# Kernel tuning notes

Hardware: AMD Instinct MI355X
Metric: run time of the kernel (lower is better)

## Reference

```python
import jax, jax.numpy as jnp
import numpy as np
import math


def _conv2d(x, w, b):
    # 3x3, stride 1, pad 1, NCHW / OIHW
    y = jax.lax.conv_general_dilated(x, w, (1, 1), ((1, 1), (1, 1)),
                                     dimension_numbers=('NCHW', 'OIHW', 'NCHW'))
    return y + b[None, :, None, None]


def _avgpool2(x):
    B, C, H, W = x.shape
    return x.reshape(B, C, H // 2, 2, W // 2, 2).mean(axis=(3, 5))


def setup_inputs() -> dict:
    key = jax.random.key(0)
    ks = jax.random.split(key, 12)
    B, H, W = 8, 512, 512
    x = jax.random.uniform(ks[0], (B, 3, H, W), dtype=jnp.float32)

    def conv_w(k, o, i):
        return jax.random.normal(k, (o, i, 3, 3), jnp.float32) / jnp.sqrt(jnp.float32(i * 9))

    def lin_w(k, o, i):
        return jax.random.normal(k, (o, i), jnp.float32) / jnp.sqrt(jnp.float32(i))

    return {
        'x': x,
        'w1': conv_w(ks[1], 16, 6),  'b1': jnp.zeros((16,), jnp.float32),
        'w2': conv_w(ks[2], 32, 16), 'b2': jnp.zeros((32,), jnp.float32),
        'w3': conv_w(ks[3], 64, 32), 'b3': jnp.zeros((64,), jnp.float32),
        'fw1': lin_w(ks[4], 256, 64),  'fb1': jnp.zeros((256,), jnp.float32),
        'fw2': lin_w(ks[5], 100, 256), 'fb2': jnp.zeros((100,), jnp.float32),
    }


def reference(x, w1, b1, w2, b2, w3, b3, fw1, fb1, fw2, fb2):
    B, C, H, W = x.shape
    # radial distance from image center (torch.meshgrid default = 'ij')
    a, b = jnp.meshgrid(jnp.arange(H), jnp.arange(W), indexing='ij')
    dist = jnp.sqrt((a - H / 2) ** 2 + (b - W / 2) ** 2).astype(jnp.float32)
    max_radius = math.sqrt(H * H + W * W) / 2

    xf = jnp.fft.fftn(x, axes=(-1, -2))
    # torch.fft.fftshift with no dim shifts ALL axes (incl. B, C); jnp matches.
    xf = jnp.fft.fftshift(xf)
    x_mag = jnp.log10(jnp.abs(xf) + 1)

    fi = jnp.concatenate([x, x_mag], axis=1)  # [B,6,H,W]
    y = jax.nn.relu(_conv2d(fi, w1, b1))
    y = _avgpool2(y)
    y = jax.nn.relu(_conv2d(y, w2, b2))
    y = _avgpool2(y)
    y = _conv2d(y, w3, b3)
    y = y.mean(axis=(2, 3))  # AdaptiveAvgPool2d((1,1)) -> [B,64]
    # note: NO activation between the two FC layers in the original
    value_set = jax.nn.leaky_relu((y @ fw1.T + fb1) @ fw2.T + fb2, 0.01)  # [B,100]

    # 100 radial ring bins; replace the 100-iter where-loop with bucketize+gather
    radius_set = max_radius * (jnp.arange(100, dtype=jnp.float32) + 1.0) * 0.01
    # bin i: radius_set[i-1] < dist <= radius_set[i]  ==  searchsorted left
    bin_idx = jnp.clip(jnp.searchsorted(radius_set, dist, side='left'), 0, 99)  # [H,W]
    fq_mask = value_set[:, bin_idx]  # [B,H,W] gather, same math as sum of ring masks

    low = xf * fq_mask[:, None, :, :]
    low = jnp.fft.ifftshift(low)
    low = jnp.fft.ifftn(low, axes=(-1, -2))
    lowpass = jnp.clip(low.real, 0.0, 1.0)
    return lowpass, fq_mask, value_set
```

## Files before the change

### kernel.cpp

```cpp
#include <hip/hip_runtime.h>
#include <math.h>

#define NPIX 262144
#define FSTR 513

typedef __attribute__((ext_vector_type(2))) float v2f;

__device__ __forceinline__ int brev9(int i) { return (int)(__brev((unsigned)i) >> 23); }

__device__ __forceinline__ void init_tw(float* twr, float* twi, int t) {
  if (t < 256) {
    float ang = -3.14159265358979323846f * (float)t / 256.0f;
    float s, c;
    sincosf(ang, &s, &c);
    twr[t] = c; twi[t] = s;
  }
}

template<bool FWD>
__device__ __forceinline__ void fft512x8(float* __restrict__ sr, float* __restrict__ si,
                                         const float* __restrict__ twr,
                                         const float* __restrict__ twi, int t) {
  const int c  = t >> 5;
  const int tq = t & 31;
  float* cr = sr + c * FSTR;
  float* ci = si + c * FSTR;
  #pragma unroll
  for (int sp = 0; sp < 4; sp++) {
    const int s = 2 * sp;
    const int h = 1 << s;
    __syncthreads();
    #pragma unroll
    for (int m = 0; m < 4; m++) {
      int q = tq + 32 * m;
      int j = q & (h - 1);
      int base = ((q >> s) << (s + 2)) | j;
      int i1 = j << (8 - s);
      int i2 = j << (7 - s);
      float w1r = twr[i1], w1i = FWD ? twi[i1] : -twi[i1];
      float w2r = twr[i2], w2i = FWD ? twi[i2] : -twi[i2];
      float ar = cr[base],         ai = ci[base];
      float br = cr[base + h],     bi = ci[base + h];
      float c2r = cr[base + 2*h],  c2i = ci[base + 2*h];
      float dr = cr[base + 3*h],   di = ci[base + 3*h];
      float wbr = br * w1r - bi * w1i, wbi = br * w1i + bi * w1r;
      float wdr = dr * w1r - di * w1i, wdi = dr * w1i + di * w1r;
      float t0r = ar + wbr,  t0i = ai + wbi;
      float t1r = ar - wbr,  t1i = ai - wbi;
      float t2r = c2r + wdr, t2i = c2i + wdi;
      float t3r = c2r - wdr, t3i = c2i - wdi;
      float u2r = t2r * w2r - t2i * w2i, u2i = t2r * w2i + t2i * w2r;
      float v3r = t3r * w2r - t3i * w2i, v3i = t3r * w2i + t3i * w2r;
      float u3r = FWD ? v3i : -v3i;
      float u3i = FWD ? -v3r : v3r;
      cr[base]         = t0r + u2r;  ci[base]         = t0i + u2i;
      cr[base + 2*h]   = t0r - u2r;  ci[base + 2*h]   = t0i - u2i;
      cr[base + h]     = t1r + u3r;  ci[base + h]     = t1i + u3i;
      cr[base + 3*h]   = t1r - u3r;  ci[base + 3*h]   = t1i - u3i;
    }
  }
  __syncthreads();
  #pragma unroll
  for (int m = 0; m < 8; m++) {
    int k = tq + 32 * m;
    float wr = twr[k], wi = FWD ? twi[k] : -twi[k];
    float vr = cr[k + 256], vi = ci[k + 256];
    float tr = vr * wr - vi * wi;
    float ti = vr * wi + vi * wr;
    float ur = cr[k], ui = ci[k];
    cr[k] = ur + tr;        ci[k] = ui + ti;
    cr[k + 256] = ur - tr;  ci[k + 256] = ui - ti;
  }
  __syncthreads();
}

__global__ __launch_bounds__(256) void k_fft_rows(const float* __restrict__ x,
                                                  float2* __restrict__ xf) {
  __shared__ float sr[8 * FSTR], si[8 * FSTR], twr[256], twi[256];
  int t = threadIdx.x;
  int img = blockIdx.x >> 6;
  int r0 = (blockIdx.x & 63) << 3;
  init_tw(twr, twi, t);
  const float4* p4 = (const float4*)(x + (size_t)img * NPIX + (size_t)r0 * 512);
  for (int e = t; e < 1024; e += 256) {
    int row = e >> 7, w = e & 127;
    float4 f = p4[e];
    float* cr = sr + row * FSTR;
    float* ci = si + row * FSTR;
    int p = 4 * w;
    cr[brev9(p)]     = f.x;  ci[brev9(p)]     = 0.0f;
    cr[brev9(p + 1)] = f.y;  ci[brev9(p + 1)] = 0.0f;
    cr[brev9(p + 2)] = f.z;  ci[brev9(p + 2)] = 0.0f;
    cr[brev9(p + 3)] = f.w;  ci[brev9(p + 3)] = 0.0f;
  }
  fft512x8<true>(sr, si, twr, twi, t);
  float4* q4 = (float4*)(xf + (size_t)img * NPIX + (size_t)r0 * 512);
  for (int e = t; e < 2048; e += 256) {
    int row = e >> 8, u = e & 255;
    const float* cr = sr + row * FSTR;
    const float* ci = si + row * FSTR;
    q4[e] = make_float4(cr[2 * u], ci[2 * u], cr[2 * u + 1], ci[2 * u + 1]);
  }
}

__global__ __launch_bounds__(256) void k_fft_cols(float2* __restrict__ xf,
                                                  float* __restrict__ xmag) {
  __shared__ float sr[8 * FSTR], si[8 * FSTR], twr[256], twi[256];
  int t = threadIdx.x;
  int img = blockIdx.x >> 6;
  int c0 = (blockIdx.x & 63) << 3;
  init_tw(twr, twi, t);
  float2* base = xf + (size_t)img * NPIX + c0;
  const int q = t & 3;
  const int j = (t >> 2) & 15;
  const int w = t >> 6;
  #pragma unroll
  for (int it = 0; it < 8; it++) {
    int row = 32 * j + 4 * it + w;
    float4 f = *(const float4*)(base + (size_t)row * 512 + 2 * q);
    int rr = brev9(row);
    sr[(2 * q) * FSTR + rr]     = f.x;  si[(2 * q) * FSTR + rr]     = f.y;
    sr[(2 * q + 1) * FSTR + rr] = f.z;  si[(2 * q + 1) * FSTR + rr] = f.w;
  }
  fft512x8<true>(sr, si, twr, twi, t);
  int sb = img / 3, sc = img - 3 * sb;
  int dimg = ((sb + 4) & 7) * 3 + (sc + 1) % 3;
  float* xb = xmag + (size_t)dimg * NPIX + (c0 ^ 256);
  const int rg = t >> 2;
  #pragma unroll
  for (int it = 0; it < 8; it++) {
    int row = 64 * it + rg;
    float a0 = sr[(2 * q) * FSTR + row],     b0 = si[(2 * q) * FSTR + row];
    float a1 = sr[(2 * q + 1) * FSTR + row], b1 = si[(2 * q + 1) * FSTR + row];
    *(float4*)(base + (size_t)row * 512 + 2 * q) = make_float4(a0, b0, a1, b1);
    float m0 = log10f(sqrtf(a0 * a0 + b0 * b0) + 1.0f);
    float m1 = log10f(sqrtf(a1 * a1 + b1 * b1) + 1.0f);
    *(float2*)(xb + (size_t)(row ^ 256) * 512 + 2 * q) = make_float2(m0, m1);
  }
}

__global__ __launch_bounds__(256) void k_conv1(const float* __restrict__ x,
                                               const float* __restrict__ xmag,
                                               const float* __restrict__ w1,
                                               const float* __restrict__ b1,
                                               float* __restrict__ out) {
  __shared__ float tile[2][18 * 132 + 8];
  const int t = threadIdx.x;
  const int tx = t & 31, ty = t >> 5;
  const int PC0 = blockIdx.x * 64;
  const int PR0 = blockIdx.y * 8;
  const int b  = blockIdx.z >> 1;
  const int og = (blockIdx.z & 1) * 8;
  const int R0 = PR0 * 2 - 1;
  const int C0 = PC0 * 2 - 1;

  int li[10], gi[10];
  bool okf[10];
  #pragma unroll
  for (int k = 0; k < 10; k++) {
    int e = t + 256 * k;
    bool valid = e < 2340;
    int i = e / 130, j = e - i * 130;
    int rr = R0 + i, cc = C0 + j;
    bool ok = valid && ((unsigned)rr < 512u) && ((unsigned)cc < 512u);
    li[k] = valid ? (i * 132 + j) : (18 * 132);
    gi[k] = ok ? (rr * 512 + cc) : 0;
    okf[k] = ok;
  }

  v2f acc[8][4];
  #pragma unroll
  for (int o = 0; o < 8; o++)
    #pragma unroll
    for (int q = 0; q < 4; q++) acc[o][q] = (v2f){0.0f, 0.0f};

  const float* xb = x + (size_t)(b * 3) * NPIX;
  const float* mb = xmag + (size_t)(b * 3) * NPIX;

  float ld[10];
  #pragma unroll
  for (int k = 0; k < 10; k++) ld[k] = okf[k] ? xb[gi[k]] : 0.0f;
  #pragma unroll
  for (int k = 0; k < 10; k++) tile[0][li[k]] = ld[k];
  __syncthreads();

  for (int ic = 0; ic < 6; ic++) {
    if (ic < 5) {
      const float* sn = (ic + 1 < 3) ? (xb + (size_t)(ic + 1) * NPIX)
                                     : (mb + (size_t)(ic - 2) * NPIX);
      #pragma unroll
      for (int k = 0; k < 10; k++) ld[k] = okf[k] ? sn[gi[k]] : 0.0f;
    }
    const float* cur = tile[ic & 1];
    float patch[4][6];
    #pragma unroll
    for (int dy = 0; dy < 4; dy++) {
      const float* rp = cur + (2 * ty + dy) * 132 + 4 * tx;
      float4 f = *(const float4*)rp;
      float2 g = *(const float2*)(rp + 4);
      patch[dy][0] = f.x; patch[dy][1] = f.y; patch[dy][2] = f.z;
      patch[dy][3] = f.w; patch[dy][4] = g.x; patch[dy][5] = g.y;
    }
    v2f pr[4][5];
    #pragma unroll
    for (int dy = 0; dy < 4; dy++)
      #pragma unroll
      for (int s = 0; s < 5; s++)
        pr[dy][s] = (v2f){patch[dy][s], patch[dy][s + 1]};
    #pragma unroll
    for (int o = 0; o < 8; o++) {
      const float* wk = w1 + (size_t)((og + o) * 6 + ic) * 9;
      #pragma unroll
      for (int dy = 0; dy < 3; dy++)
        #pragma unroll
        for (int kc = 0; kc < 3; kc++) {
          float kw = wk[dy * 3 + kc];
          v2f wv = (v2f){kw, kw};
          acc[o][0] += wv * pr[dy][kc];
          acc[o][1] += wv * pr[dy][kc + 2];
          acc[o][2] += wv * pr[dy + 1][kc];
          acc[o][3] += wv * pr[dy + 1][kc + 2];
        }
    }
    if (ic < 5) {
      float* nxt = tile[(ic + 1) & 1];
      #pragma unroll
      for (int k = 0; k < 10; k++) nxt[li[k]] = ld[k];
      __syncthreads();
    }
  }
  #pragma unroll
  for (int o = 0; o < 8; o++) {
    float bias = b1[og + o];
    float p0 = fmaxf(acc[o][0].x + bias, 0.0f) + fmaxf(acc[o][0].y + bias, 0.0f)
             + fmaxf(acc[o][2].x + bias, 0.0f) + fmaxf(acc[o][2].y + bias, 0.0f);
    float p1 = fmaxf(acc[o][1].x + bias, 0.0f) + fmaxf(acc[o][1].y + bias, 0.0f)
             + fmaxf(acc[o][3].x + bias, 0.0f) + fmaxf(acc[o][3].y + bias, 0.0f);
    float2* q = (float2*)(out + ((size_t)(b * 16 + og + o) * 256 + PR0 + ty) * 256 + PC0 + 2 * tx);
    *q = make_float2(p0 * 0.25f, p1 * 0.25f);
  }
}

__global__ __launch_bounds__(256) void k_conv2(const float* __restrict__ in,
                                               const float* __restrict__ w2,
                                               const float* __restrict__ b2,
                                               float* __restrict__ S) {
  __shared__ float tile[2][18 * 68 + 8];
  __shared__ float wsum[4][8];
  const int t = threadIdx.x;
  const int tx = t & 31, ty = t >> 5;
  const int bx = blockIdx.x, by = blockIdx.y;
  const int PC0 = bx * 32;
  const int PR0 = by * 8;
  const int b  = blockIdx.z >> 2;
  const int og = (blockIdx.z & 3) * 8;
  const int R0 = PR0 * 2 - 1;
  const int C0 = PC0 * 2 - 1;

  int li[5], gi[5];
  bool okf[5];
  #pragma unroll
  for (int k = 0; k < 5; k++) {
    int e = t + 256 * k;
    bool valid = e < 1188;
    int i = e / 66, j = e - 66 * i;
    int rr = R0 + i, cc = C0 + j;
    bool ok = valid && ((unsigned)rr < 256u) && ((unsigned)cc < 256u);
    li[k] = valid ? (i * 68 + j) : (18 * 68);
    gi[k] = ok ? (rr * 256 + cc) : 0;
    okf[k] = ok;
  }

  v2f acc[8][2];
  #pragma unroll
  for (int o = 0; o < 8; o++) {
    acc[o][0] = (v2f){0.0f, 0.0f};
    acc[o][1] = (v2f){0.0f, 0.0f};
  }

  const float* inb = in + (size_t)(b * 16) * 65536;

  float ld[5];
  #pragma unroll
  for (int k = 0; k < 5; k++) ld[k] = okf[k] ? inb[gi[k]] : 0.0f;
  #pragma unroll
  for (int k = 0; k < 5; k++) tile[0][li[k]] = ld[k];
  __syncthreads();

  for (int ic = 0; ic < 16; ic++) {
    if (ic < 15) {
      const float* sn = inb + (size_t)(ic + 1) * 65536;
      #pragma unroll
      for (int k = 0; k < 5; k++) ld[k] = okf[k] ? sn[gi[k]] : 0.0f;
    }
    const float* cur = tile[ic & 1];
    float patch[4][4];
    #pragma unroll
    for (int dy = 0; dy < 4; dy++) {
      const float* rp = cur + (2 * ty + dy) * 68 + 2 * tx;
      float2 f0 = *(const float2*)rp;
      float2 f1 = *(const float2*)(rp + 2);
      patch[dy][0] = f0.x; patch[dy][1] = f0.y;
      patch[dy][2] = f1.x; patch[dy][3] = f1.y;
    }
    v2f pr[4][3];
    #pragma unroll
    for (int dy = 0; dy < 4; dy++) {
      pr[dy][0] = (v2f){patch[dy][0], patch[dy][1]};
      pr[dy][1] = (v2f){patch[dy][1], patch[dy][2]};
      pr[dy][2] = (v2f){patch[dy][2], patch[dy][3]};
    }
    #pragma unroll
    for (int o = 0; o < 8; o++) {
      const float* wk = w2 + (size_t)((og + o) * 16 + ic) * 9;
      #pragma unroll
      for (int dy = 0; dy < 3; dy++)
        #pragma unroll
        for (int kc = 0; kc < 3; kc++) {
          float kw = wk[dy * 3 + kc];
          v2f wv = (v2f){kw, kw};
          acc[o][0] += wv * pr[dy][kc];
          acc[o][1] += wv * pr[dy + 1][kc];
        }
    }
    if (ic < 15) {
      float* nxt = tile[(ic + 1) & 1];
      #pragma unroll
      for (int k = 0; k < 5; k++) nxt[li[k]] = ld[k];
      __syncthreads();
    }
  }

  const int lane = t & 63;
  const int wid = t >> 6;
  float* Sb0 = S + (size_t)(b * 32 + og) * 9;
  #pragma unroll
  for (int o = 0; o < 8; o++) {
    float bias = b2[og + o];
    float v = (fmaxf(acc[o][0].x + bias, 0.0f) + fmaxf(acc[o][0].y + bias, 0.0f)
             + fmaxf(acc[o][1].x + bias, 0.0f) + fmaxf(acc[o][1].y + bias, 0.0f)) * 0.25f;
    float* Sb = Sb0 + o * 9;
    float ts = v;
    #pragma unroll
    for (int off = 32; off > 0; off >>= 1) ts += __shfl_down(ts, off);
    if (lane == 0) wsum[wid][o] = ts;
    if (by == 0) {
      float e = (ty == 0) ? v : 0.0f;
      #pragma unroll
      for (int off = 32; off > 0; off >>= 1) e += __shfl_down(e, off);
      if (lane == 0) atomicAdd(&Sb[1], e);
    }
    if (by == 15) {
      float e = (ty == 7) ? v : 0.0f;
      #pragma unroll
      for (int off = 32; off > 0; off >>= 1) e += __shfl_down(e, off);
      if (lane == 0) atomicAdd(&Sb[2], e);
    }
    if (bx == 0 && tx == 0)  atomicAdd(&Sb[3], v);
    if (bx == 3 && tx == 31) atomicAdd(&Sb[4], v);
    if (bx == 0 && by == 0  && t == 0)   Sb[5] = v;
    if (bx == 3 && by == 0  && t == 31)  Sb[6] = v;
    if (bx == 0 && by == 15 && t == 224) Sb[7] = v;
    if (bx == 3 && by == 15 && t == 255) Sb[8] = v;
  }
  __syncthreads();
  if (t < 8)
    atomicAdd(&Sb0[t * 9], wsum[0][t] + wsum[1][t] + wsum[2][t] + wsum[3][t]);
}

__global__ __launch_bounds__(256) void k_fc(const float* __restrict__ S,
                                            const float* __restrict__ w3,
                                            const float* __restrict__ b3,
                                            const float* __restrict__ fw1,
                                            const float* __restrict__ fb1,
                                            const float* __restrict__ fw2,
                                            const float* __restrict__ fb2,
                                            float* __restrict__ vs_out) {
  __shared__ float Sp[2304];
  __shared__ float y[512];
  __shared__ float h1[2048];
  int t = threadIdx.x;
  for (int e = t; e < 2304; e += 256) {
    int cell = e / 9, k = e - 9 * cell;
    int dy = k / 3, dx = k - 3 * dy;
    const float* s = S + cell * 9;
    float v = s[0];
    if (dy == 0) v -= s[2];
    if (dy == 2) v -= s[1];
    if (dx == 0) v -= s[4];
    if (dx == 2) v -= s[3];
    if (dy == 0 && dx == 0) v += s[8];
    if (dy == 0 && dx == 2) v += s[7];
    if (dy == 2 && dx == 0) v += s[6];
    if (dy == 2 && dx == 2) v += s[5];
    Sp[e] = v;
  }
  __syncthreads();
  for (int e = t; e < 512; e += 256) {
    int b = e >> 6, o = e & 63;
    const float* wrow = w3 + (size_t)o * 288;
    const float* sp = Sp + b * 288;
    float s = 0.0f;
    #pragma unroll 4
    for (int k = 0; k < 288; k++) s += wrow[k] * sp[k];
    y[e] = b3[o] + s * (1.0f / 16384.0f);
  }
  __syncthreads();
  for (int e = t; e < 2048; e += 256) {
    int b = e >> 8, j = e & 255;
    float s = fb1[j];
    for (int k = 0; k < 64; k++) s += y[b * 64 + k] * fw1[j * 64 + k];
    h1[e] = s;
  }
  __syncthreads();
  for (int e = t; e < 800; e += 256) {
    int b = e / 100, i = e - 100 * b;
    float s = fb2[i];
    for (int j = 0; j < 256; j++) s += h1[b * 256 + j] * fw2[i * 256 + j];
    vs_out[e] = (s >= 0.0f) ? s : 0.01f * s;
  }
}

__global__ __launch_bounds__(256) void k_mask(const float* __restrict__ vs,
                                              float* __restrict__ fq_mask) {
  int idx = blockIdx.x * 256 + threadIdx.x;
  int h = idx >> 9, w = idx & 511;
  float da = (float)h - 256.0f, db = (float)w - 256.0f;
  float dist = sqrtf(da * da + db * db);
  int lo = 0, hi = 100;
  while (lo < hi) {
    int mid = (lo + hi) >> 1;
    float r = (362.03867196751236f * (float)(mid + 1)) * 0.01f;
    if (r < dist) lo = mid + 1; else hi = mid;
  }
  int bin = lo > 99 ? 99 : lo;
  #pragma unroll
  for (int b = 0; b < 8; b++)
    fq_mask[(size_t)b * NPIX + idx] = vs[b * 100 + bin];
}

__global__ __launch_bounds__(256) void k_ifft_rows_mod(float2* __restrict__ xf,
                                                       const float* __restrict__ fq_mask) {
  __shared__ float sr[8 * FSTR], si[8 * FSTR], twr[256], twi[256];
  int t = threadIdx.x;
  int img = blockIdx.x >> 6;
  int r0 = (blockIdx.x & 63) << 3;
  int bm = ((img / 3) + 4) & 7;
  init_tw(twr, twi, t);
  const float* mbase = fq_mask + (size_t)bm * NPIX;
  float4* base4 = (float4*)(xf + (size_t)img * NPIX + (size_t)r0 * 512);
  for (int e = t; e < 2048; e += 256) {
    int u = (e & 3) | (((e >> 2) & 15) << 3) | (((e >> 6) & 1) << 2) | (((e >> 7) & 1) << 7);
    int row = e >> 8;
    float4 f = base4[row * 256 + u];
    int p0 = 2 * u;
    const float* mrow = mbase + (size_t)((r0 + row + 256) & 511) * 512;
    float2 m = *(const float2*)(mrow + ((p0 + 256) & 511));
    int rr0 = brev9(p0);
    float* cr = sr + row * FSTR;
    float* ci = si + row * FSTR;
    cr[rr0]       = f.x * m.x;  ci[rr0]       = f.y * m.x;
    cr[rr0 + 256] = f.z * m.y;  ci[rr0 + 256] = f.w * m.y;
  }
  fft512x8<false>(sr, si, twr, twi, t);
  for (int e = t; e < 2048; e += 256) {
    int row = e >> 8, u = e & 255;
    const float* cr = sr + row * FSTR;
    const float* ci = si + row * FSTR;
    base4[e] = make_float4(cr[2 * u], ci[2 * u], cr[2 * u + 1], ci[2 * u + 1]);
  }
}

__global__ __launch_bounds__(256) void k_ifft_cols_out(const float2* __restrict__ xf,
                                                       float* __restrict__ lowpass) {
  __shared__ float sr[8 * FSTR], si[8 * FSTR], twr[256], twi[256];
  int t = threadIdx.x;
  int img = blockIdx.x >> 6;
  int c0 = (blockIdx.x & 63) << 3;
  init_tw(twr, twi, t);
  const float2* base = xf + (size_t)img * NPIX + c0;
  const int q = t & 3;
  const int j = (t >> 2) & 15;
  const int w = t >> 6;
  #pragma unroll
  for (int it = 0; it < 8; it++) {
    int row = 32 * j + 4 * it + w;
    float4 f = *(const float4*)(base + (size_t)row * 512 + 2 * q);
    int rr = brev9(row);
    sr[(2 * q) * FSTR + rr]     = f.x;  si[(2 * q) * FSTR + rr]     = f.y;
    sr[(2 * q + 1) * FSTR + rr] = f.z;  si[(2 * q + 1) * FSTR + rr] = f.w;
  }
  fft512x8<false>(sr, si, twr, twi, t);
  const float sc = 1.0f / 262144.0f;
  float* obase = lowpass + (size_t)img * NPIX + c0;
  const int rg = t >> 2;
  #pragma unroll
  for (int it = 0; it < 8; it++) {
    int row = 64 * it + rg;
    float v0 = fminf(fmaxf(sr[(2 * q) * FSTR + row] * sc, 0.0f), 1.0f);
    float v1 = fminf(fmaxf(sr[(2 * q + 1) * FSTR + row] * sc, 0.0f), 1.0f);
    *(float2*)(obase + (size_t)row * 512 + 2 * q) = make_float2(v0, v1);
  }
}

extern "C" void kernel_launch(void* const* d_in, const int* in_sizes, int n_in,
                              void* d_out, int out_size, void* d_ws, size_t ws_size,
                              hipStream_t stream) {
  const float* x   = (const float*)d_in[0];
  const float* w1  = (const float*)d_in[1];
  const float* b1  = (const float*)d_in[2];
  const float* w2  = (const float*)d_in[3];
  const float* b2  = (const float*)d_in[4];
  const float* w3  = (const float*)d_in[5];
  const float* b3  = (const float*)d_in[6];
  const float* fw1 = (const float*)d_in[7];
  const float* fb1 = (const float*)d_in[8];
  const float* fw2 = (const float*)d_in[9];
  const float* fb2 = (const float*)d_in[10];

  float* lowpass = (float*)d_out;
  float* fq_mask = lowpass + 6291456;
  float* vs      = fq_mask + 2097152;

  float* base    = (float*)d_ws;
  float2* xf     = (float2*)base;
  float* xmag    = base + 12582912;
  float* pooled1 = xmag + 6291456;
  float* S       = pooled1 + 8388608;

  k_fft_rows<<<dim3(24 * 64), 256, 0, stream>>>(x, xf);
  k_fft_cols<<<dim3(24 * 64), 256, 0, stream>>>(xf, xmag);

  k_conv1<<<dim3(4, 32, 16), 256, 0, stream>>>(x, xmag, w1, b1, pooled1);
  hipMemsetAsync(S, 0, 2304 * sizeof(float), stream);
  k_conv2<<<dim3(4, 16, 32), 256, 0, stream>>>(pooled1, w2, b2, S);

  k_fc<<<1, 256, 0, stream>>>(S, w3, b3, fw1, fb1, fw2, fb2, vs);
  k_mask<<<1024, 256, 0, stream>>>(vs, fq_mask);

  k_ifft_rows_mod<<<dim3(24 * 64), 256, 0, stream>>>(xf, fq_mask);
  k_ifft_cols_out<<<dim3(24 * 64), 256, 0, stream>>>(xf, lowpass);
}
```

Baseline: 393.6 us.

## Pack pairs of real images into one complex FFT to halve FFT work

Two real input images are packed as the real and imaginary parts of one complex signal, so forward and inverse 2D FFTs run on 12 images instead of 24. A new kernel separates the two spectra through Hermitian symmetry to compute the log magnitudes. The inverse row pass applies the two images' masks to the packed spectrum, and the final column pass writes real and imaginary parts as two outputs. The cost is an extra separation kernel and scattered mirrored reads, plus a second spectrum buffer because the mask step now reads mirrored entries and cannot update in place.

```diff
diff --git a/kernel.cpp b/kernel.cpp
--- a/kernel.cpp
+++ b/kernel.cpp
@@ -5,6 +5,7 @@
 #define FSTR 513
 
 typedef __attribute__((ext_vector_type(2))) float v2f;
+
 
 __device__ __forceinline__ int brev9(int i) { return (int)(__brev((unsigned)i) >> 23); }
 
@@ -74,27 +75,36 @@
   __syncthreads();
 }
 
+__device__ __forceinline__ void pair_src(int p, int& ia, int& ib) {
+  if (p < 8) { ia = 3 * p; ib = 3 * p + 1; }
+  else { int k = p - 8; ia = 6 * k + 2; ib = 6 * k + 5; }
+}
+
 __global__ __launch_bounds__(256) void k_fft_rows(const float* __restrict__ x,
                                                   float2* __restrict__ xf) {
   __shared__ float sr[8 * FSTR], si[8 * FSTR], twr[256], twi[256];
   int t = threadIdx.x;
-  int img = blockIdx.x >> 6;
+  int p = blockIdx.x >> 6;
   int r0 = (blockIdx.x & 63) << 3;
   init_tw(twr, twi, t);
-  const float4* p4 = (const float4*)(x + (size_t)img * NPIX + (size_t)r0 * 512);
+  int ia, ib;
+  pair_src(p, ia, ib);
+  const float4* pa = (const float4*)(x + (size_t)ia * NPIX + (size_t)r0 * 512);
+  const float4* pb = (const float4*)(x + (size_t)ib * NPIX + (size_t)r0 * 512);
   for (int e = t; e < 1024; e += 256) {
     int row = e >> 7, w = e & 127;
-    float4 f = p4[e];
+    float4 fa = pa[e];
+    float4 fb = pb[e];
     float* cr = sr + row * FSTR;
     float* ci = si + row * FSTR;
-    int p = 4 * w;
-    cr[brev9(p)]     = f.x;  ci[brev9(p)]     = 0.0f;
-    cr[brev9(p + 1)] = f.y;  ci[brev9(p + 1)] = 0.0f;
-    cr[brev9(p + 2)] = f.z;  ci[brev9(p + 2)] = 0.0f;
-    cr[brev9(p + 3)] = f.w;  ci[brev9(p + 3)] = 0.0f;
+    int pc = 4 * w;
+    cr[brev9(pc)]     = fa.x;  ci[brev9(pc)]     = fb.x;
+    cr[brev9(pc + 1)] = fa.y;  ci[brev9(pc + 1)] = fb.y;
+    cr[brev9(pc + 2)] = fa.z;  ci[brev9(pc + 2)] = fb.z;
+    cr[brev9(pc + 3)] = fa.w;  ci[brev9(pc + 3)] = fb.w;
   }
   fft512x8<true>(sr, si, twr, twi, t);
-  float4* q4 = (float4*)(xf + (size_t)img * NPIX + (size_t)r0 * 512);
+  float4* q4 = (float4*)(xf + (size_t)p * NPIX + (size_t)r0 * 512);
   for (int e = t; e < 2048; e += 256) {
     int row = e >> 8, u = e & 255;
     const float* cr = sr + row * FSTR;
@@ -103,14 +113,13 @@
   }
 }
 
-__global__ __launch_bounds__(256) void k_fft_cols(float2* __restrict__ xf,
-                                                  float* __restrict__ xmag) {
+__global__ __launch_bounds__(256) void k_fft_cols(float2* __restrict__ xf) {
   __shared__ float sr[8 * FSTR], si[8 * FSTR], twr[256], twi[256];
   int t = threadIdx.x;
-  int img = blockIdx.x >> 6;
+  int p = blockIdx.x >> 6;
   int c0 = (blockIdx.x & 63) << 3;
   init_tw(twr, twi, t);
-  float2* base = xf + (size_t)img * NPIX + c0;
+  float2* base = xf + (size_t)p * NPIX + c0;
   const int q = t & 3;
   const int j = (t >> 2) & 15;
   const int w = t >> 6;
@@ -123,9 +132,6 @@
     sr[(2 * q + 1) * FSTR + rr] = f.z;  si[(2 * q + 1) * FSTR + rr] = f.w;
   }
   fft512x8<true>(sr, si, twr, twi, t);
-  int sb = img / 3, sc = img - 3 * sb;
-  int dimg = ((sb + 4) & 7) * 3 + (sc + 1) % 3;
-  float* xb = xmag + (size_t)dimg * NPIX + (c0 ^ 256);
   const int rg = t >> 2;
   #pragma unroll
   for (int it = 0; it < 8; it++) {
@@ -133,9 +139,45 @@
     float a0 = sr[(2 * q) * FSTR + row],     b0 = si[(2 * q) * FSTR + row];
     float a1 = sr[(2 * q + 1) * FSTR + row], b1 = si[(2 * q + 1) * FSTR + row];
     *(float4*)(base + (size_t)row * 512 + 2 * q) = make_float4(a0, b0, a1, b1);
-    float m0 = log10f(sqrtf(a0 * a0 + b0 * b0) + 1.0f);
-    float m1 = log10f(sqrtf(a1 * a1 + b1 * b1) + 1.0f);
-    *(float2*)(xb + (size_t)(row ^ 256) * 512 + 2 * q) = make_float2(m0, m1);
+  }
+}
+
+__global__ __launch_bounds__(256) void k_xmag(const float2* __restrict__ xf,
+                                              float* __restrict__ xmag) {
+  int t = threadIdx.x;
+  int p = blockIdx.x >> 6;
+  int r0 = (blockIdx.x & 63) << 3;
+  int da, db;
+  if (p < 8) {
+    int bs = (p + 4) & 7;
+    da = bs * 3 + 1;
+    db = bs * 3 + 2;
+  } else {
+    int k = p - 8;
+    da = ((2 * k + 4) & 7) * 3;
+    db = ((2 * k + 5) & 7) * 3;
+  }
+  const float2* Z = xf + (size_t)p * NPIX;
+  float* A = xmag + (size_t)da * NPIX;
+  float* B = xmag + (size_t)db * NPIX;
+  for (int e = t; e < 2048; e += 256) {
+    int row = r0 + (e >> 8);
+    int c0 = (e & 255) * 2;
+    float4 z01 = *(const float4*)(Z + (size_t)row * 512 + c0);
+    int mr = (512 - row) & 511;
+    float2 zm0 = Z[(size_t)mr * 512 + ((512 - c0) & 511)];
+    float2 zm1 = Z[(size_t)mr * 512 + (511 - c0)];
+    float ar0 = 0.5f * (z01.x + zm0.x), ai0 = 0.5f * (z01.y - zm0.y);
+    float br0 = 0.5f * (z01.x - zm0.x), bi0 = 0.5f * (z01.y + zm0.y);
+    float ar1 = 0.5f * (z01.z + zm1.x), ai1 = 0.5f * (z01.w - zm1.y);
+    float br1 = 0.5f * (z01.z - zm1.x), bi1 = 0.5f * (z01.w + zm1.y);
+    float ma0 = log10f(sqrtf(ar0 * ar0 + ai0 * ai0) + 1.0f);
+    float ma1 = log10f(sqrtf(ar1 * ar1 + ai1 * ai1) + 1.0f);
+    float mb0 = log10f(sqrtf(br0 * br0 + bi0 * bi0) + 1.0f);
+    float mb1 = log10f(sqrtf(br1 * br1 + bi1 * bi1) + 1.0f);
+    size_t off = (size_t)(row ^ 256) * 512 + (c0 ^ 256);
+    *(float2*)(A + off) = make_float2(ma0, ma1);
+    *(float2*)(B + off) = make_float2(mb0, mb1);
   }
 }
 
@@ -439,46 +481,79 @@
     fq_mask[(size_t)b * NPIX + idx] = vs[b * 100 + bin];
 }
 
-__global__ __launch_bounds__(256) void k_ifft_rows_mod(float2* __restrict__ xf,
+__global__ __launch_bounds__(256) void k_ifft_rows_mod(const float2* __restrict__ xf,
+                                                       float2* __restrict__ xf2,
                                                        const float* __restrict__ fq_mask) {
   __shared__ float sr[8 * FSTR], si[8 * FSTR], twr[256], twi[256];
   int t = threadIdx.x;
-  int img = blockIdx.x >> 6;
+  int p = blockIdx.x >> 6;
   int r0 = (blockIdx.x & 63) << 3;
-  int bm = ((img / 3) + 4) & 7;
   init_tw(twr, twi, t);
-  const float* mbase = fq_mask + (size_t)bm * NPIX;
-  float4* base4 = (float4*)(xf + (size_t)img * NPIX + (size_t)r0 * 512);
-  for (int e = t; e < 2048; e += 256) {
-    int u = (e & 3) | (((e >> 2) & 15) << 3) | (((e >> 6) & 1) << 2) | (((e >> 7) & 1) << 7);
-    int row = e >> 8;
-    float4 f = base4[row * 256 + u];
-    int p0 = 2 * u;
-    const float* mrow = mbase + (size_t)((r0 + row + 256) & 511) * 512;
-    float2 m = *(const float2*)(mrow + ((p0 + 256) & 511));
-    int rr0 = brev9(p0);
-    float* cr = sr + row * FSTR;
-    float* ci = si + row * FSTR;
-    cr[rr0]       = f.x * m.x;  ci[rr0]       = f.y * m.x;
-    cr[rr0 + 256] = f.z * m.y;  ci[rr0 + 256] = f.w * m.y;
+  if (p < 8) {
+    int bm = (p + 4) & 7;
+    const float* mbase = fq_mask + (size_t)bm * NPIX;
+    const float4* base4 = (const float4*)(xf + (size_t)p * NPIX + (size_t)r0 * 512);
+    for (int e = t; e < 2048; e += 256) {
+      int u = (e & 3) | (((e >> 2) & 15) << 3) | (((e >> 6) & 1) << 2) | (((e >> 7) & 1) << 7);
+      int row = e >> 8;
+      float4 f = base4[row * 256 + u];
+      int p0 = 2 * u;
+      const float* mrow = mbase + (size_t)((r0 + row + 256) & 511) * 512;
+      float2 m = *(const float2*)(mrow + ((p0 + 256) & 511));
+      int rr0 = brev9(p0);
+      float* cr = sr + row * FSTR;
+      float* ci = si + row * FSTR;
+      cr[rr0]       = f.x * m.x;  ci[rr0]       = f.y * m.x;
+      cr[rr0 + 256] = f.z * m.y;  ci[rr0 + 256] = f.w * m.y;
+    }
+  } else {
+    int k = p - 8;
+    const float* fa = fq_mask + (size_t)((2 * k + 4) & 7) * NPIX;
+    const float* fb = fq_mask + (size_t)((2 * k + 5) & 7) * NPIX;
+    const float2* Z = xf + (size_t)p * NPIX;
+    for (int e = t; e < 2048; e += 256) {
+      int row = e >> 8;
+      int gr = r0 + row;
+      int c0 = (e & 255) * 2;
+      float4 z01 = *(const float4*)(Z + (size_t)gr * 512 + c0);
+      int mr = (512 - gr) & 511;
+      float2 zm0 = Z[(size_t)mr * 512 + ((512 - c0) & 511)];
+      float2 zm1 = Z[(size_t)mr * 512 + (511 - c0)];
+      size_t mro = (size_t)((gr + 256) & 511) * 512;
+      int mc = (c0 + 256) & 511;
+      float2 ma = *(const float2*)(fa + mro + mc);
+      float2 mb = *(const float2*)(fb + mro + mc);
+      float s0 = 0.5f * (ma.x + mb.x), d0 = 0.5f * (ma.x - mb.x);
+      float s1 = 0.5f * (ma.y + mb.y), d1 = 0.5f * (ma.y - mb.y);
+      float wr0 = s0 * z01.x + d0 * zm0.x;
+      float wi0 = s0 * z01.y - d0 * zm0.y;
+      float wr1 = s1 * z01.z + d1 * zm1.x;
+      float wi1 = s1 * z01.w - d1 * zm1.y;
+      int rr0 = brev9(c0);
+      float* cr = sr + row * FSTR;
+      float* ci = si + row * FSTR;
+      cr[rr0]       = wr0;  ci[rr0]       = wi0;
+      cr[rr0 + 256] = wr1;  ci[rr0 + 256] = wi1;
+    }
   }
   fft512x8<false>(sr, si, twr, twi, t);
+  float4* o4 = (float4*)(xf2 + (size_t)p * NPIX + (size_t)r0 * 512);
   for (int e = t; e < 2048; e += 256) {
     int row = e >> 8, u = e & 255;
     const float* cr = sr + row * FSTR;
     const float* ci = si + row * FSTR;
-    base4[e] = make_float4(cr[2 * u], ci[2 * u], cr[2 * u + 1], ci[2 * u + 1]);
-  }
-}
-
-__global__ __launch_bounds__(256) void k_ifft_cols_out(const float2* __restrict__ xf,
+    o4[e] = make_float4(cr[2 * u], ci[2 * u], cr[2 * u + 1], ci[2 * u + 1]);
+  }
+}
+
+__global__ __launch_bounds__(256) void k_ifft_cols_out(const float2* __restrict__ xf2,
                                                        float* __restrict__ lowpass) {
   __shared__ float sr[8 * FSTR], si[8 * FSTR], twr[256], twi[256];
   int t = threadIdx.x;
-  int img = blockIdx.x >> 6;
+  int p = blockIdx.x >> 6;
   int c0 = (blockIdx.x & 63) << 3;
   init_tw(twr, twi, t);
-  const float2* base = xf + (size_t)img * NPIX + c0;
+  const float2* base = xf2 + (size_t)p * NPIX + c0;
   const int q = t & 3;
   const int j = (t >> 2) & 15;
   const int w = t >> 6;
@@ -492,14 +567,22 @@
   }
   fft512x8<false>(sr, si, twr, twi, t);
   const float sc = 1.0f / 262144.0f;
-  float* obase = lowpass + (size_t)img * NPIX + c0;
+  int ia, ib;
+  pair_src(p, ia, ib);
+  float* oa = lowpass + (size_t)ia * NPIX + c0;
+  float* ob = lowpass + (size_t)ib * NPIX + c0;
   const int rg = t >> 2;
   #pragma unroll
   for (int it = 0; it < 8; it++) {
     int row = 64 * it + rg;
-    float v0 = fminf(fmaxf(sr[(2 * q) * FSTR + row] * sc, 0.0f), 1.0f);
-    float v1 = fminf(fmaxf(sr[(2 * q + 1) * FSTR + row] * sc, 0.0f), 1.0f);
-    *(float2*)(obase + (size_t)row * 512 + 2 * q) = make_float2(v0, v1);
+    float re0 = sr[(2 * q) * FSTR + row],     im0 = si[(2 * q) * FSTR + row];
+    float re1 = sr[(2 * q + 1) * FSTR + row], im1 = si[(2 * q + 1) * FSTR + row];
+    float a0 = fminf(fmaxf(re0 * sc, 0.0f), 1.0f);
+    float a1 = fminf(fmaxf(re1 * sc, 0.0f), 1.0f);
+    float b0 = fminf(fmaxf(im0 * sc, 0.0f), 1.0f);
+    float b1 = fminf(fmaxf(im1 * sc, 0.0f), 1.0f);
+    *(float2*)(oa + (size_t)row * 512 + 2 * q) = make_float2(a0, a1);
+    *(float2*)(ob + (size_t)row * 512 + 2 * q) = make_float2(b0, b1);
   }
 }
 
@@ -524,12 +607,14 @@
 
   float* base    = (float*)d_ws;
   float2* xf     = (float2*)base;
+  float2* xf2    = (float2*)(base + 6291456);
   float* xmag    = base + 12582912;
   float* pooled1 = xmag + 6291456;
   float* S       = pooled1 + 8388608;
 
-  k_fft_rows<<<dim3(24 * 64), 256, 0, stream>>>(x, xf);
-  k_fft_cols<<<dim3(24 * 64), 256, 0, stream>>>(xf, xmag);
+  k_fft_rows<<<dim3(12 * 64), 256, 0, stream>>>(x, xf);
+  k_fft_cols<<<dim3(12 * 64), 256, 0, stream>>>(xf);
+  k_xmag<<<dim3(12 * 64), 256, 0, stream>>>(xf, xmag);
 
   k_conv1<<<dim3(4, 32, 16), 256, 0, stream>>>(x, xmag, w1, b1, pooled1);
   hipMemsetAsync(S, 0, 2304 * sizeof(float), stream);
@@ -538,6 +623,6 @@
   k_fc<<<1, 256, 0, stream>>>(S, w3, b3, fw1, fb1, fw2, fb2, vs);
   k_mask<<<1024, 256, 0, stream>>>(vs, fq_mask);
 
-  k_ifft_rows_mod<<<dim3(24 * 64), 256, 0, stream>>>(xf, fq_mask);
-  k_ifft_cols_out<<<dim3(24 * 64), 256, 0, stream>>>(xf, lowpass);
-}
+  k_ifft_rows_mod<<<dim3(12 * 64), 256, 0, stream>>>(xf, xf2, fq_mask);
+  k_ifft_cols_out<<<dim3(12 * 64), 256, 0, stream>>>(xf2, lowpass);
+}
```

Result: faster. 358.1 us (-9.0%).
